# Kernel optimization log

Hardware: AMD Instinct MI355X
Metric: run time of the kernel (lower is better)

Reference implementation:

```python
import jax, jax.numpy as jnp
import numpy as np

STATE_DIM = 128
NUM_STATES = 16
BATCH = 16384


def setup_inputs() -> dict:
    key = jax.random.key(0)
    k1, k2, k3, k4 = jax.random.split(key, 4)
    x = jax.random.normal(k1, (BATCH, STATE_DIM), dtype=jnp.float32)
    state_idx = jax.random.randint(k2, (BATCH,), 0, NUM_STATES)
    A_all = jax.random.normal(k3, (NUM_STATES, STATE_DIM, STATE_DIM), dtype=jnp.float32)
    C_all = jax.random.normal(k4, (NUM_STATES, STATE_DIM, STATE_DIM), dtype=jnp.float32)
    return {"x": x, "state_idx": state_idx, "A_all": A_all, "C_all": C_all}


def reference(x, state_idx, A_all, C_all):
    # Per-sample expert matrix gather: [B, D, D]
    Ag = A_all[state_idx]
    Cg = C_all[state_idx]
    # state = relu(x @ A_i) per sample, batched via einsum
    state = jax.nn.relu(jnp.einsum('bd,bde->be', x, Ag))
    # observation = state @ C_i
    out = jnp.einsum('be,bef->bf', state, Cg)
    return out
```

## Files before the change

### kernel.cpp

```cpp
#include <hip/hip_runtime.h>

#define D 128
#define NS 16
#define BATCH 16384
#define TILE 32
#define CHUNK 512
#define NCH (BATCH / CHUNK)

typedef __attribute__((ext_vector_type(8))) short short8;
typedef __attribute__((ext_vector_type(4))) float f32x4;

__device__ __forceinline__ unsigned short f2bf(float f) {
  unsigned u = __builtin_bit_cast(unsigned, f);
  u += 0x7FFFu + ((u >> 16) & 1u);
  return (unsigned short)(u >> 16);
}

__global__ __launch_bounds__(256) void prep_kernel(
    const float* __restrict__ A_all, const float* __restrict__ C_all,
    unsigned short* __restrict__ At, unsigned short* __restrict__ Ct) {
  const int b = blockIdx.x, tid = threadIdx.x;
  __shared__ float T[32][129];
  const int mat = b >> 6, r = b & 63, s = r >> 2, slab = r & 3;
  const float* in = (mat ? C_all : A_all) + (size_t)s * D * D;
  unsigned short* outp = (mat ? Ct : At) + (size_t)s * D * D;
  const int e0 = slab * 32;
  const int ecol = (tid & 7) * 4;
  const int drow = tid >> 3;
#pragma unroll
  for (int i = 0; i < 4; i++) {
    const int d = drow + 32 * i;
    const float4 v = *(const float4*)(in + (size_t)d * D + e0 + ecol);
    T[ecol + 0][d] = v.x;
    T[ecol + 1][d] = v.y;
    T[ecol + 2][d] = v.z;
    T[ecol + 3][d] = v.w;
  }
  __syncthreads();
  const int e = tid >> 3;
  const int d0 = (tid & 7) * 16;
  unsigned short p[16];
#pragma unroll
  for (int k = 0; k < 16; k++) p[k] = f2bf(T[e][d0 + k]);
  unsigned short* dst = outp + (size_t)(e0 + e) * D + d0;
  *(uint4*)(dst) = *(const uint4*)(p);
  *(uint4*)(dst + 8) = *(const uint4*)(p + 8);
}

__global__ __launch_bounds__(256, 2) void ssm_kernel(
    const float* __restrict__ x,
    const int* __restrict__ sidx,
    const unsigned short* __restrict__ At,
    const unsigned short* __restrict__ Ct,
    float* __restrict__ out) {
  __shared__ unsigned short Xs[TILE][136];
  __shared__ unsigned short Hs[TILE][136];
  __shared__ unsigned short Ws[D][136];
  __shared__ int rowlist[CHUNK];
  __shared__ int wcnt[8];

  const int s = blockIdx.y;
  const int c0 = blockIdx.x * CHUNK;
  const int tid = threadIdx.x;
  const int lane = tid & 63, w = tid >> 6;
  const int l15 = lane & 15, quad = lane >> 4;
  const int wr = w & 1, wc = w >> 1;

  uint4 atr[8], ctr[8];
  {
    const uint4* gA = (const uint4*)(At + (size_t)s * D * D);
    const uint4* gC = (const uint4*)(Ct + (size_t)s * D * D);
#pragma unroll
    for (int i = 0; i < 8; i++) { atr[i] = gA[i * 256 + tid]; ctr[i] = gC[i * 256 + tid]; }
  }

  const int v0 = sidx[c0 + tid];
  const int v1 = sidx[c0 + 256 + tid];
  const unsigned long long lanelt = (1ull << lane) - 1ull;
  const unsigned long long m0 = __ballot(v0 == s);
  const unsigned long long m1 = __ballot(v1 == s);
  if (lane == 0) { wcnt[w] = (int)__popcll(m0); wcnt[4 + w] = (int)__popcll(m1); }
  __syncthreads();
  int pre0 = 0, pre1 = 0, tot0 = 0, cnt = 0;
#pragma unroll
  for (int ww = 0; ww < 4; ww++) {
    if (ww < w) { pre0 += wcnt[ww]; pre1 += wcnt[4 + ww]; }
    tot0 += wcnt[ww];
    cnt += wcnt[ww] + wcnt[4 + ww];
  }
  if (v0 == s) rowlist[pre0 + (int)__popcll(m0 & lanelt)] = c0 + tid;
  if (v1 == s) rowlist[tot0 + pre1 + (int)__popcll(m1 & lanelt)] = c0 + 256 + tid;
  __syncthreads();

  for (int i0 = 0; i0 < cnt; i0 += TILE) {
    if (i0) __syncthreads();

#pragma unroll
    for (int i = 0; i < 8; i++) {
      const int c = i * 256 + tid;
      *(uint4*)&Ws[c >> 4][(c & 15) * 8] = atr[i];
    }
    {
      const int r = tid >> 3, q = tid & 7;
      const int rl = i0 + r;
      const int rid = (rl < cnt) ? rowlist[rl] : -1;
      unsigned short* xr = &Xs[r][q * 16];
      if (rid >= 0) {
        const float4* src = (const float4*)(x + (size_t)rid * D + q * 16);
#pragma unroll
        for (int i = 0; i < 4; i++) {
          float4 v = src[i];
          ushort4 p;
          p.x = f2bf(v.x); p.y = f2bf(v.y); p.z = f2bf(v.z); p.w = f2bf(v.w);
          *(ushort4*)(xr + i * 4) = p;
        }
      } else {
        ushort4 z; z.x = z.y = z.z = z.w = 0;
#pragma unroll
        for (int i = 0; i < 4; i++) *(ushort4*)(xr + i * 4) = z;
      }
    }
    __syncthreads();

    f32x4 acc[4];
#pragma unroll
    for (int nb = 0; nb < 4; nb++) acc[nb] = (f32x4){0.f, 0.f, 0.f, 0.f};
#pragma unroll
    for (int kb = 0; kb < 4; kb++) {
      short8 aF = *(const short8*)&Xs[wr * 16 + l15][kb * 32 + quad * 8];
#pragma unroll
      for (int nb = 0; nb < 4; nb++) {
        short8 bF = *(const short8*)&Ws[wc * 64 + nb * 16 + l15][kb * 32 + quad * 8];
        acc[nb] = __builtin_amdgcn_mfma_f32_16x16x32_bf16(aF, bF, acc[nb], 0, 0, 0);
      }
    }
#pragma unroll
    for (int nb = 0; nb < 4; nb++)
#pragma unroll
      for (int rr = 0; rr < 4; rr++) {
        float v = acc[nb][rr];
        Hs[wr * 16 + quad * 4 + rr][wc * 64 + nb * 16 + l15] = f2bf(v > 0.f ? v : 0.f);
      }
    __syncthreads();

#pragma unroll
    for (int i = 0; i < 8; i++) {
      const int c = i * 256 + tid;
      *(uint4*)&Ws[c >> 4][(c & 15) * 8] = ctr[i];
    }
    __syncthreads();

#pragma unroll
    for (int nb = 0; nb < 4; nb++) acc[nb] = (f32x4){0.f, 0.f, 0.f, 0.f};
#pragma unroll
    for (int kb = 0; kb < 4; kb++) {
      short8 aF = *(const short8*)&Hs[wr * 16 + l15][kb * 32 + quad * 8];
#pragma unroll
      for (int nb = 0; nb < 4; nb++) {
        short8 bF = *(const short8*)&Ws[wc * 64 + nb * 16 + l15][kb * 32 + quad * 8];
        acc[nb] = __builtin_amdgcn_mfma_f32_16x16x32_bf16(aF, bF, acc[nb], 0, 0, 0);
      }
    }

#pragma unroll
    for (int rr = 0; rr < 4; rr++) {
      const int rl = wr * 16 + quad * 4 + rr;
      if (i0 + rl < cnt) {
        float* orow = out + (size_t)rowlist[i0 + rl] * D + wc * 64 + l15;
#pragma unroll
        for (int nb = 0; nb < 4; nb++) orow[nb * 16] = acc[nb][rr];
      }
    }
  }
}

extern "C" void kernel_launch(void* const* d_in, const int* in_sizes, int n_in,
                              void* d_out, int out_size, void* d_ws, size_t ws_size,
                              hipStream_t stream) {
  const float* x = (const float*)d_in[0];
  const int* sidx = (const int*)d_in[1];
  const float* A_all = (const float*)d_in[2];
  const float* C_all = (const float*)d_in[3];
  float* out = (float*)d_out;

  unsigned short* At = (unsigned short*)d_ws;
  unsigned short* Ct = At + NS * D * D;

  prep_kernel<<<128, 256, 0, stream>>>(A_all, C_all, At, Ct);
  ssm_kernel<<<dim3(NCH, NS), 256, 0, stream>>>(x, sidx, At, Ct, out);
}
```

Before: 88.40 us.

## Fuse weight transpose/convert into main kernel and double row tile

Removes the separate prep kernel; each block now transposes and converts its expert's A and C from fp32 to bf16 in shared memory, reusing the weight buffer as a transpose scratch. The row tile is doubled to 64 with each wave computing two 16-row MFMA tiles, and blocks with no rows exit early. This saves a kernel launch and workspace traffic but makes every block redo the conversion and read fp32 weights, and the larger tile adds more padding for the typical ~32 rows per block.

New measurement: 79.16 us. 10.5% less time.

```diff
diff --git a/kernel.cpp b/kernel.cpp
--- a/kernel.cpp
+++ b/kernel.cpp
@@ -3,7 +3,7 @@
 #define D 128
 #define NS 16
 #define BATCH 16384
-#define TILE 32
+#define TILE 64
 #define CHUNK 512
 #define NCH (BATCH / CHUNK)
 
@@ -16,46 +16,17 @@
   return (unsigned short)(u >> 16);
 }
 
-__global__ __launch_bounds__(256) void prep_kernel(
-    const float* __restrict__ A_all, const float* __restrict__ C_all,
-    unsigned short* __restrict__ At, unsigned short* __restrict__ Ct) {
-  const int b = blockIdx.x, tid = threadIdx.x;
-  __shared__ float T[32][129];
-  const int mat = b >> 6, r = b & 63, s = r >> 2, slab = r & 3;
-  const float* in = (mat ? C_all : A_all) + (size_t)s * D * D;
-  unsigned short* outp = (mat ? Ct : At) + (size_t)s * D * D;
-  const int e0 = slab * 32;
-  const int ecol = (tid & 7) * 4;
-  const int drow = tid >> 3;
-#pragma unroll
-  for (int i = 0; i < 4; i++) {
-    const int d = drow + 32 * i;
-    const float4 v = *(const float4*)(in + (size_t)d * D + e0 + ecol);
-    T[ecol + 0][d] = v.x;
-    T[ecol + 1][d] = v.y;
-    T[ecol + 2][d] = v.z;
-    T[ecol + 3][d] = v.w;
-  }
-  __syncthreads();
-  const int e = tid >> 3;
-  const int d0 = (tid & 7) * 16;
-  unsigned short p[16];
-#pragma unroll
-  for (int k = 0; k < 16; k++) p[k] = f2bf(T[e][d0 + k]);
-  unsigned short* dst = outp + (size_t)(e0 + e) * D + d0;
-  *(uint4*)(dst) = *(const uint4*)(p);
-  *(uint4*)(dst + 8) = *(const uint4*)(p + 8);
-}
-
-__global__ __launch_bounds__(256, 2) void ssm_kernel(
+__global__ __launch_bounds__(256, 2) void ssm_fused(
     const float* __restrict__ x,
     const int* __restrict__ sidx,
-    const unsigned short* __restrict__ At,
-    const unsigned short* __restrict__ Ct,
+    const float* __restrict__ A_all,
+    const float* __restrict__ C_all,
     float* __restrict__ out) {
+  __shared__ __align__(16) char smemW[D * 136 * 2];
+  unsigned short (*Ws)[136] = (unsigned short (*)[136])smemW;
+  float (*T)[129] = (float (*)[129])smemW;
   __shared__ unsigned short Xs[TILE][136];
   __shared__ unsigned short Hs[TILE][136];
-  __shared__ unsigned short Ws[D][136];
   __shared__ int rowlist[CHUNK];
   __shared__ int wcnt[8];
 
@@ -65,14 +36,6 @@
   const int lane = tid & 63, w = tid >> 6;
   const int l15 = lane & 15, quad = lane >> 4;
   const int wr = w & 1, wc = w >> 1;
-
-  uint4 atr[8], ctr[8];
-  {
-    const uint4* gA = (const uint4*)(At + (size_t)s * D * D);
-    const uint4* gC = (const uint4*)(Ct + (size_t)s * D * D);
-#pragma unroll
-    for (int i = 0; i < 8; i++) { atr[i] = gA[i * 256 + tid]; ctr[i] = gC[i * 256 + tid]; }
-  }
 
   const int v0 = sidx[c0 + tid];
   const int v1 = sidx[c0 + 256 + tid];
@@ -90,8 +53,48 @@
   }
   if (v0 == s) rowlist[pre0 + (int)__popcll(m0 & lanelt)] = c0 + tid;
   if (v1 == s) rowlist[tot0 + pre1 + (int)__popcll(m1 & lanelt)] = c0 + 256 + tid;
-  __syncthreads();
-
+  if (cnt == 0) return;
+
+  uint4 atr[8], ctr[8];
+  {
+    const float* __restrict__ srcA = A_all + (size_t)s * D * D;
+    const float* __restrict__ srcC = C_all + (size_t)s * D * D;
+    const int ecol = (tid & 7) * 4;
+    const int drow = tid >> 3;
+#pragma unroll
+    for (int mat = 0; mat < 2; mat++) {
+      const float* __restrict__ src = mat ? srcC : srcA;
+#pragma unroll
+      for (int sl = 0; sl < 4; sl++) {
+        const int e0 = sl * 32;
+        __syncthreads();
+#pragma unroll
+        for (int i = 0; i < 4; i++) {
+          const int d = drow + 32 * i;
+          const float4 v = *(const float4*)(src + (size_t)d * D + e0 + ecol);
+          T[ecol + 0][d] = v.x;
+          T[ecol + 1][d] = v.y;
+          T[ecol + 2][d] = v.z;
+          T[ecol + 3][d] = v.w;
+        }
+        __syncthreads();
+#pragma unroll
+        for (int ii = 0; ii < 2; ii++) {
+          const int c = (2 * sl + ii) * 256 + tid;
+          const int e = (c >> 4) - e0;
+          const int d0 = (c & 15) * 8;
+          unsigned short p[8];
+#pragma unroll
+          for (int k = 0; k < 8; k++) p[k] = f2bf(T[e][d0 + k]);
+          if (mat) ctr[2 * sl + ii] = *(const uint4*)p;
+          else     atr[2 * sl + ii] = *(const uint4*)p;
+        }
+      }
+    }
+    __syncthreads();
+  }
+
+#pragma unroll 1
   for (int i0 = 0; i0 < cnt; i0 += TILE) {
     if (i0) __syncthreads();
 
@@ -101,14 +104,13 @@
       *(uint4*)&Ws[c >> 4][(c & 15) * 8] = atr[i];
     }
     {
-      const int r = tid >> 3, q = tid & 7;
-      const int rl = i0 + r;
-      const int rid = (rl < cnt) ? rowlist[rl] : -1;
-      unsigned short* xr = &Xs[r][q * 16];
+      const int r = tid >> 2, q = tid & 3;
+      const int rid = (i0 + r < cnt) ? rowlist[i0 + r] : -1;
+      unsigned short* xr = &Xs[r][q * 32];
       if (rid >= 0) {
-        const float4* src = (const float4*)(x + (size_t)rid * D + q * 16);
-#pragma unroll
-        for (int i = 0; i < 4; i++) {
+        const float4* src = (const float4*)(x + (size_t)rid * D + q * 32);
+#pragma unroll
+        for (int i = 0; i < 8; i++) {
           float4 v = src[i];
           ushort4 p;
           p.x = f2bf(v.x); p.y = f2bf(v.y); p.z = f2bf(v.z); p.w = f2bf(v.w);
@@ -117,30 +119,37 @@
       } else {
         ushort4 z; z.x = z.y = z.z = z.w = 0;
 #pragma unroll
-        for (int i = 0; i < 4; i++) *(ushort4*)(xr + i * 4) = z;
-      }
-    }
-    __syncthreads();
-
-    f32x4 acc[4];
-#pragma unroll
-    for (int nb = 0; nb < 4; nb++) acc[nb] = (f32x4){0.f, 0.f, 0.f, 0.f};
+        for (int i = 0; i < 8; i++) *(ushort4*)(xr + i * 4) = z;
+      }
+    }
+    __syncthreads();
+
+    f32x4 acc[2][4];
+#pragma unroll
+    for (int ti = 0; ti < 2; ti++)
+#pragma unroll
+      for (int nb = 0; nb < 4; nb++) acc[ti][nb] = (f32x4){0.f, 0.f, 0.f, 0.f};
 #pragma unroll
     for (int kb = 0; kb < 4; kb++) {
-      short8 aF = *(const short8*)&Xs[wr * 16 + l15][kb * 32 + quad * 8];
+      short8 aF0 = *(const short8*)&Xs[(wr * 2 + 0) * 16 + l15][kb * 32 + quad * 8];
+      short8 aF1 = *(const short8*)&Xs[(wr * 2 + 1) * 16 + l15][kb * 32 + quad * 8];
 #pragma unroll
       for (int nb = 0; nb < 4; nb++) {
         short8 bF = *(const short8*)&Ws[wc * 64 + nb * 16 + l15][kb * 32 + quad * 8];
-        acc[nb] = __builtin_amdgcn_mfma_f32_16x16x32_bf16(aF, bF, acc[nb], 0, 0, 0);
-      }
-    }
-#pragma unroll
-    for (int nb = 0; nb < 4; nb++)
-#pragma unroll
-      for (int rr = 0; rr < 4; rr++) {
-        float v = acc[nb][rr];
-        Hs[wr * 16 + quad * 4 + rr][wc * 64 + nb * 16 + l15] = f2bf(v > 0.f ? v : 0.f);
-      }
+        acc[0][nb] = __builtin_amdgcn_mfma_f32_16x16x32_bf16(aF0, bF, acc[0][nb], 0, 0, 0);
+        acc[1][nb] = __builtin_amdgcn_mfma_f32_16x16x32_bf16(aF1, bF, acc[1][nb], 0, 0, 0);
+      }
+    }
+#pragma unroll
+    for (int ti = 0; ti < 2; ti++)
+#pragma unroll
+      for (int nb = 0; nb < 4; nb++)
+#pragma unroll
+        for (int rr = 0; rr < 4; rr++) {
+          float v = acc[ti][nb][rr];
+          Hs[(wr * 2 + ti) * 16 + quad * 4 + rr][wc * 64 + nb * 16 + l15] =
+              f2bf(v > 0.f ? v : 0.f);
+        }
     __syncthreads();
 
 #pragma unroll
@@ -151,26 +160,32 @@
     __syncthreads();
 
 #pragma unroll
-    for (int nb = 0; nb < 4; nb++) acc[nb] = (f32x4){0.f, 0.f, 0.f, 0.f};
+    for (int ti = 0; ti < 2; ti++)
+#pragma unroll
+      for (int nb = 0; nb < 4; nb++) acc[ti][nb] = (f32x4){0.f, 0.f, 0.f, 0.f};
 #pragma unroll
     for (int kb = 0; kb < 4; kb++) {
-      short8 aF = *(const short8*)&Hs[wr * 16 + l15][kb * 32 + quad * 8];
+      short8 aF0 = *(const short8*)&Hs[(wr * 2 + 0) * 16 + l15][kb * 32 + quad * 8];
+      short8 aF1 = *(const short8*)&Hs[(wr * 2 + 1) * 16 + l15][kb * 32 + quad * 8];
 #pragma unroll
       for (int nb = 0; nb < 4; nb++) {
         short8 bF = *(const short8*)&Ws[wc * 64 + nb * 16 + l15][kb * 32 + quad * 8];
-        acc[nb] = __builtin_amdgcn_mfma_f32_16x16x32_bf16(aF, bF, acc[nb], 0, 0, 0);
-      }
-    }
-
-#pragma unroll
-    for (int rr = 0; rr < 4; rr++) {
-      const int rl = wr * 16 + quad * 4 + rr;
-      if (i0 + rl < cnt) {
-        float* orow = out + (size_t)rowlist[i0 + rl] * D + wc * 64 + l15;
-#pragma unroll
-        for (int nb = 0; nb < 4; nb++) orow[nb * 16] = acc[nb][rr];
-      }
-    }
+        acc[0][nb] = __builtin_amdgcn_mfma_f32_16x16x32_bf16(aF0, bF, acc[0][nb], 0, 0, 0);
+        acc[1][nb] = __builtin_amdgcn_mfma_f32_16x16x32_bf16(aF1, bF, acc[1][nb], 0, 0, 0);
+      }
+    }
+
+#pragma unroll
+    for (int ti = 0; ti < 2; ti++)
+#pragma unroll
+      for (int rr = 0; rr < 4; rr++) {
+        const int rl = (wr * 2 + ti) * 16 + quad * 4 + rr;
+        if (i0 + rl < cnt) {
+          float* orow = out + (size_t)rowlist[i0 + rl] * D + wc * 64 + l15;
+#pragma unroll
+          for (int nb = 0; nb < 4; nb++) orow[nb * 16] = acc[ti][nb][rr];
+        }
+      }
   }
 }
 
@@ -183,9 +198,5 @@
   const float* C_all = (const float*)d_in[3];
   float* out = (float*)d_out;
 
-  unsigned short* At = (unsigned short*)d_ws;
-  unsigned short* Ct = At + NS * D * D;
-
-  prep_kernel<<<128, 256, 0, stream>>>(A_all, C_all, At, Ct);
-  ssm_kernel<<<dim3(NCH, NS), 256, 0, stream>>>(x, sidx, At, Ct, out);
+  ssm_fused<<<dim3(NCH, NS), 256, 0, stream>>>(x, sidx, A_all, C_all, out);
 }
```
